# Performance work log

Hardware: AMD Instinct MI355X
Metric: run time of the kernel (lower is better)

## Reference

```python
import jax, jax.numpy as jnp
import numpy as np
import math

NUM_HEADS = 16
NUM_KV_HEADS = 4
HEAD_DIM = 128
ROPE_THETA = 10000.0


def rotate_half(x):
    half = x.shape[-1] // 2
    return jnp.concatenate((-x[..., half:], x[..., :half]), axis=-1)


def setup_inputs() -> dict:
    key = jax.random.key(0)
    ks = jax.random.split(key, 5)
    B, S, H = 2, 2048, 2048
    hidden_states = jax.random.normal(ks[0], (B, S, H), dtype=jnp.float32)
    scale = 1.0 / math.sqrt(H)
    wq = jax.random.normal(ks[1], (NUM_HEADS * HEAD_DIM, H), dtype=jnp.float32) * scale
    wk = jax.random.normal(ks[2], (NUM_KV_HEADS * HEAD_DIM, H), dtype=jnp.float32) * scale
    wv = jax.random.normal(ks[3], (NUM_KV_HEADS * HEAD_DIM, H), dtype=jnp.float32) * scale
    wo = jax.random.normal(ks[4], (H, NUM_HEADS * HEAD_DIM), dtype=jnp.float32) * scale
    # additive causal mask [B,1,S,S]
    causal = jnp.where(jnp.tril(jnp.ones((S, S), dtype=bool)), 0.0, -1e9).astype(jnp.float32)
    attention_mask = jnp.broadcast_to(causal[None, None], (B, 1, S, S))
    position_ids = jnp.broadcast_to(jnp.arange(S, dtype=jnp.int64)[None], (B, S))
    return {
        'hidden_states': hidden_states, 'wq': wq, 'wk': wk, 'wv': wv, 'wo': wo,
        'attention_mask': attention_mask, 'position_ids': position_ids,
    }


def reference(hidden_states, wq, wk, wv, wo, attention_mask, position_ids):
    B, S, H = hidden_states.shape
    nh, nkv, hd = NUM_HEADS, NUM_KV_HEADS, HEAD_DIM
    groups = nh // nkv

    # projections (torch Linear: x @ W^T)
    q = (hidden_states @ wq.T).reshape(B, S, nh, hd).transpose(0, 2, 1, 3)   # [B,nh,S,hd]
    k = (hidden_states @ wk.T).reshape(B, S, nkv, hd).transpose(0, 2, 1, 3)  # [B,nkv,S,hd]
    v = (hidden_states @ wv.T).reshape(B, S, nkv, hd).transpose(0, 2, 1, 3)

    # RoPE: cos/sin gathered by position_ids -> [B,1,S,hd]
    inv_freq = 1.0 / (ROPE_THETA ** (jnp.arange(0, hd, 2, dtype=jnp.float32) / hd))  # [hd/2]
    freqs = position_ids.astype(jnp.float32)[:, :, None] * inv_freq                  # [B,S,hd/2]
    emb = jnp.concatenate((freqs, freqs), axis=-1)                                   # [B,S,hd]
    cos = jnp.cos(emb)[:, None]
    sin = jnp.sin(emb)[:, None]
    q = q * cos + rotate_half(q) * sin
    k = k * cos + rotate_half(k) * sin

    # GQA: repeat kv heads
    k = jnp.repeat(k, groups, axis=1)  # [B,nh,S,hd]
    v = jnp.repeat(v, groups, axis=1)

    scores = jnp.einsum('bhqd,bhkd->bhqk', q, k) / math.sqrt(hd) + attention_mask
    attn = jax.nn.softmax(scores.astype(jnp.float32), axis=-1).astype(q.dtype)
    ctx = jnp.einsum('bhqk,bhkd->bhqd', attn, v)            # [B,nh,S,hd]
    ctx = ctx.transpose(0, 2, 1, 3).reshape(B, S, nh * hd)  # [B,S,H]
    out = ctx @ wo.T
    return out
```

## Files before the change

### kernel.cpp

```cpp
#include <hip/hip_runtime.h>
#include <hip/hip_bf16.h>
#include <stdint.h>

typedef __bf16 bf16x8 __attribute__((ext_vector_type(8)));
typedef float f32x4 __attribute__((ext_vector_type(4)));
typedef float f32x16 __attribute__((ext_vector_type(16)));

#define NH 16
#define NKV 4
#define HD 128
#define HQ (NH*HD)
#define HKV (NKV*HD)
#define LDX 3072

__device__ __forceinline__ void gl_lds16(const void* g, void* l) {
  __builtin_amdgcn_global_load_lds(
      (const __attribute__((address_space(1))) void*)g,
      (__attribute__((address_space(3))) void*)l, 16, 0, 0);
}

__device__ __forceinline__ uint32_t pk2(float lo, float hi) {
  union { __hip_bfloat16 h[2]; uint32_t u; } x;
  x.h[0] = __float2bfloat16(lo);
  x.h[1] = __float2bfloat16(hi);
  return x.u;
}

__global__ void k_cast_all(const float* __restrict__ hs, const float* __restrict__ wq,
                           const float* __restrict__ wk, const float* __restrict__ wv,
                           const float* __restrict__ wo,
                           __hip_bfloat16* __restrict__ Xb, __hip_bfloat16* __restrict__ Wqb,
                           __hip_bfloat16* __restrict__ Wkb, __hip_bfloat16* __restrict__ Wvb,
                           __hip_bfloat16* __restrict__ Wob) {
  int i = blockIdx.x * blockDim.x + threadIdx.x;
  const float* src; __hip_bfloat16* dst; int off;
  if (i < 2097152)      { src = hs; dst = Xb;  off = i; }
  else if (i < 3145728) { src = wq; dst = Wqb; off = i - 2097152; }
  else if (i < 3407872) { src = wk; dst = Wkb; off = i - 3145728; }
  else if (i < 3670016) { src = wv; dst = Wvb; off = i - 3407872; }
  else                  { src = wo; dst = Wob; off = i - 3670016; }
  float4 v = reinterpret_cast<const float4*>(src)[off];
  union { __hip_bfloat16 b[4]; ushort4 u; } o;
  o.b[0] = __float2bfloat16(v.x); o.b[1] = __float2bfloat16(v.y);
  o.b[2] = __float2bfloat16(v.z); o.b[3] = __float2bfloat16(v.w);
  reinterpret_cast<ushort4*>(dst)[off] = o.u;
}

__global__ void k_rope_vt(__hip_bfloat16* __restrict__ X, __hip_bfloat16* __restrict__ Vt,
                          const int* __restrict__ pid, int S) {
  __shared__ __hip_bfloat16 tile[32][33];
  const int RB = 20480;
  if (blockIdx.x < RB) {
    int idx = blockIdx.x * 256 + threadIdx.x;
    int i = idx & 63;
    int hh = (idx >> 6) % 20;
    int tok = idx / (20 * 64);
    bool is64 = (pid[1] == 0);
    int pos = is64 ? pid[2 * tok] : pid[tok];
    float f = (float)pos * __expf(-(float)i * (9.210340371976184f / 64.0f));
    float sn, cs;
    __sincosf(f, &sn, &cs);
    size_t base = (size_t)tok * LDX + hh * 128;
    float x0 = __bfloat162float(X[base + i]);
    float x1 = __bfloat162float(X[base + 64 + i]);
    X[base + i]      = __float2bfloat16(x0 * cs - x1 * sn);
    X[base + 64 + i] = __float2bfloat16(x1 * cs + x0 * sn);
  } else {
    int bb = blockIdx.x - RB;
    int bkv = bb >> 8;
    int rem = bb & 255;
    int s0 = (rem & 63) * 32, d0 = (rem >> 6) * 32;
    int b = bkv >> 2, kvh = bkv & 3;
    int tx = threadIdx.x & 31, ty = threadIdx.x >> 5;
    for (int i = 0; i < 32; i += 8)
      tile[ty + i][tx] = X[((size_t)(b * S) + s0 + ty + i) * LDX + 2560 + kvh * 128 + d0 + tx];
    __syncthreads();
    for (int i = 0; i < 32; i += 8)
      Vt[((size_t)bkv * 128 + d0 + ty + i) * S + s0 + tx] = tile[tx][ty + i];
  }
}

__global__ __launch_bounds__(512, 2) void k_gemm256(
    const __hip_bfloat16* __restrict__ A,
    const __hip_bfloat16* __restrict__ Bq,
    const __hip_bfloat16* __restrict__ Bk,
    const __hip_bfloat16* __restrict__ Bv,
    __hip_bfloat16* __restrict__ C, int Nld, int K, int nbm) {
  __shared__ __hip_bfloat16 As[2][2][256 * 32];
  __shared__ __hip_bfloat16 Bs[2][2][256 * 32];

  const int t = threadIdx.x, w = t >> 6, l = t & 63;
  const int lr = l & 15, lg = l >> 4;
  const int wr = w >> 2, wc = w & 3;

  const int nwg = gridDim.x;
  const int bid = blockIdx.x;
  const int cpx = nwg >> 3;
  const int id2 = (bid & 7) * cpx + (bid >> 3);
  const int bm = id2 % nbm, bn = id2 / nbm;

  const __hip_bfloat16* Ap = A + (size_t)(bm * 256) * K;
  const __hip_bfloat16* Bp;
  if (bn < 8)       Bp = Bq + (size_t)(bn * 256) * K;
  else if (bn < 10) Bp = Bk + (size_t)((bn - 8) * 256) * K;
  else              Bp = Bv + (size_t)((bn - 10) * 256) * K;

  auto stageHalf = [&](const __hip_bfloat16* gp, __hip_bfloat16* lp, int kt, int kk) {
#pragma unroll
    for (int inst = 0; inst < 2; ++inst) {
      const int chunk = inst * 512 + t;
      const int row = chunk >> 2, c = chunk & 3;
      gl_lds16(gp + (size_t)row * K + kt * 64 + kk * 32 + c * 8,
               lp + (size_t)(inst * 512 + (w << 6)) * 8);
    }
  };

  f32x4 acc[8][4] = {};
  const int nt = K >> 6;

  stageHalf(Ap, As[0][0], 0, 0);
  stageHalf(Bp, Bs[0][0], 0, 0);
  stageHalf(Ap, As[0][1], 0, 1);
  stageHalf(Bp, Bs[0][1], 0, 1);
  stageHalf(Ap, As[1][0], 1, 0);
  stageHalf(Bp, Bs[1][0], 1, 0);
  asm volatile("s_waitcnt vmcnt(4)" ::: "memory");
  __builtin_amdgcn_s_barrier();
  asm volatile("" ::: "memory");

  for (int tt = 0; tt < nt; ++tt) {
    const int cur = tt & 1;
    const int nx1 = (tt + 1 < nt) ? tt + 1 : nt - 1;
    const int nx2 = (tt + 2 < nt) ? tt + 2 : nt - 1;
    bf16x8 bF[4];
#pragma unroll
    for (int ph = 0; ph < 4; ++ph) {
      const int kk = ph >> 1, mh = ph & 1;
      bf16x8 aF[4];
      if (mh == 0) {
#pragma unroll
        for (int n = 0; n < 4; ++n)
          bF[n] = *reinterpret_cast<const bf16x8*>(
              &Bs[cur][kk][(wc * 64 + n * 16 + lr) * 32 + lg * 8]);
      }
#pragma unroll
      for (int m = 0; m < 4; ++m)
        aF[m] = *reinterpret_cast<const bf16x8*>(
            &As[cur][kk][(wr * 128 + mh * 64 + m * 16 + lr) * 32 + lg * 8]);
      if (ph == 0)      stageHalf(Ap, As[nx1 & 1][1], nx1, 1);
      else if (ph == 1) stageHalf(Bp, Bs[nx1 & 1][1], nx1, 1);
      else if (ph == 2) stageHalf(Ap, As[nx2 & 1][0], nx2, 0);
      else              stageHalf(Bp, Bs[nx2 & 1][0], nx2, 0);
      asm volatile("" ::: "memory");
      __builtin_amdgcn_s_barrier();
      asm volatile("" ::: "memory");
      __builtin_amdgcn_s_setprio(1);
#pragma unroll
      for (int m = 0; m < 4; ++m)
#pragma unroll
        for (int n = 0; n < 4; ++n)
          acc[mh * 4 + m][n] = __builtin_amdgcn_mfma_f32_16x16x32_bf16(
              aF[m], bF[n], acc[mh * 4 + m][n], 0, 0, 0);
      __builtin_amdgcn_s_setprio(0);
      if (ph == 3) asm volatile("s_waitcnt vmcnt(4)" ::: "memory");
      asm volatile("" ::: "memory");
      __builtin_amdgcn_s_barrier();
      asm volatile("" ::: "memory");
    }
  }

  const int row0 = bm * 256 + wr * 128;
  const int col0 = bn * 256 + wc * 64;
#pragma unroll
  for (int m = 0; m < 8; ++m)
#pragma unroll
    for (int n = 0; n < 4; ++n)
#pragma unroll
      for (int r = 0; r < 4; ++r)
        C[(size_t)(row0 + m * 16 + lg * 4 + r) * Nld + col0 + n * 16 + lr] =
            __float2bfloat16(acc[m][n][r]);
}

__global__ __launch_bounds__(512, 1) void k_gemmO(
    const __hip_bfloat16* __restrict__ A, const __hip_bfloat16* __restrict__ B,
    float* __restrict__ C, int N, int K) {
  __shared__ __hip_bfloat16 As[2][2][128 * 32];
  __shared__ __hip_bfloat16 Bs[2][2][256 * 32];

  const int t = threadIdx.x, w = t >> 6, l = t & 63;
  const int lr = l & 15, lg = l >> 4;
  const int wr = w >> 2, wc = w & 3;

  const int bid = blockIdx.x;
  const int id2 = (bid & 7) * 32 + (bid >> 3);
  const int bm = id2 & 31, bn = id2 >> 5;

  const __hip_bfloat16* Ap = A + (size_t)(bm * 128) * K;
  const __hip_bfloat16* Bp = B + (size_t)(bn * 256) * K;

  auto stageA = [&](__hip_bfloat16* lp, int kt, int kk) {
    const int row = t >> 2, c = t & 3;
    gl_lds16(Ap + (size_t)row * K + kt * 64 + kk * 32 + c * 8,
             lp + (size_t)(w << 6) * 8);
  };
  auto stageB = [&](__hip_bfloat16* lp, int kt, int kk) {
#pragma unroll
    for (int inst = 0; inst < 2; ++inst) {
      const int chunk = inst * 512 + t;
      const int row = chunk >> 2, c = chunk & 3;
      gl_lds16(Bp + (size_t)row * K + kt * 64 + kk * 32 + c * 8,
               lp + (size_t)(inst * 512 + (w << 6)) * 8);
    }
  };

  f32x4 acc[4][4] = {};
  const int nt = K >> 6;

  stageA(As[0][0], 0, 0);
  stageB(Bs[0][0], 0, 0);
  stageA(As[0][1], 0, 1);
  stageB(Bs[0][1], 0, 1);
  stageA(As[1][0], 1, 0);
  stageB(Bs[1][0], 1, 0);
  asm volatile("s_waitcnt vmcnt(3)" ::: "memory");
  __builtin_amdgcn_s_barrier();
  asm volatile("" ::: "memory");

  for (int tt = 0; tt < nt; ++tt) {
    const int cur = tt & 1;
    const int nx1 = (tt + 1 < nt) ? tt + 1 : nt - 1;
    const int nx2 = (tt + 2 < nt) ? tt + 2 : nt - 1;
    bf16x8 bF[4];
#pragma unroll
    for (int ph = 0; ph < 4; ++ph) {
      const int kk = ph >> 1, mh = ph & 1;
      bf16x8 aF[2];
      if (mh == 0) {
#pragma unroll
        for (int n = 0; n < 4; ++n)
          bF[n] = *reinterpret_cast<const bf16x8*>(
              &Bs[cur][kk][(wc * 64 + n * 16 + lr) * 32 + lg * 8]);
      }
#pragma unroll
      for (int m2 = 0; m2 < 2; ++m2)
        aF[m2] = *reinterpret_cast<const bf16x8*>(
            &As[cur][kk][(wr * 64 + mh * 32 + m2 * 16 + lr) * 32 + lg * 8]);
      if (ph == 0)      stageA(As[nx1 & 1][1], nx1, 1);
      else if (ph == 1) stageB(Bs[nx1 & 1][1], nx1, 1);
      else if (ph == 2) stageA(As[nx2 & 1][0], nx2, 0);
      else              stageB(Bs[nx2 & 1][0], nx2, 0);
      asm volatile("" ::: "memory");
      __builtin_amdgcn_s_barrier();
      asm volatile("" ::: "memory");
      __builtin_amdgcn_s_setprio(1);
#pragma unroll
      for (int m2 = 0; m2 < 2; ++m2)
#pragma unroll
        for (int n = 0; n < 4; ++n)
          acc[mh * 2 + m2][n] = __builtin_amdgcn_mfma_f32_16x16x32_bf16(
              aF[m2], bF[n], acc[mh * 2 + m2][n], 0, 0, 0);
      __builtin_amdgcn_s_setprio(0);
      if (ph == 3) asm volatile("s_waitcnt vmcnt(3)" ::: "memory");
      asm volatile("" ::: "memory");
      __builtin_amdgcn_s_barrier();
      asm volatile("" ::: "memory");
    }
  }

  const int row0 = bm * 128 + wr * 64;
  const int col0 = bn * 256 + wc * 64;
#pragma unroll
  for (int m = 0; m < 4; ++m)
#pragma unroll
    for (int n = 0; n < 4; ++n)
#pragma unroll
      for (int r = 0; r < 4; ++r)
        C[(size_t)(row0 + m * 16 + lg * 4 + r) * N + col0 + n * 16 + lr] =
            acc[m][n][r];
}

__global__ __launch_bounds__(256, 2) void k_attn(
    const __hip_bfloat16* __restrict__ X, const __hip_bfloat16* __restrict__ Vt,
    __hip_bfloat16* __restrict__ ctx, int S) {
  __shared__ __hip_bfloat16 SM[32768];

  const int bid = blockIdx.x;
  const int g  = bid & 7;
  const int idx = bid >> 3;
  int hi, jj;
  if (idx < 32) { hi = idx >> 4;              jj = idx & 15; }
  else          { hi = 2 + ((idx - 32) >> 4); jj = 15 - ((idx - 32) & 15); }
  const int b = g >> 2, kvh = g & 3;
  const int h = kvh * 4 + hi;

  const int t = threadIdx.x, w = t >> 6, l = t & 63;
  const int q = l & 31, hf = l >> 5;
  const int qt64 = (w < 2) ? jj : (31 - jj);
  const int q0w = qt64 * 64 + (w & 1) * 32;
  const int nt = 32 - jj;
  const float c1 = 0.12752511f;
  const float M0 = 48.0f;

  const __hip_bfloat16* Qp = X + ((size_t)(b * S) + q0w + q) * LDX + h * 128 + hf * 8;
  bf16x8 aq[8];
#pragma unroll
  for (int m = 0; m < 8; ++m)
    aq[m] = *reinterpret_cast<const bf16x8*>(Qp + m * 16);

  const __hip_bfloat16* KG = X + (size_t)(b * S) * LDX + 2048 + kvh * 128;
  const __hip_bfloat16* VG = Vt + ((size_t)(b * NKV + kvh) * 128) * S;

  auto stageK = [&](int buf, int kv0) {
#pragma unroll
    for (int j = 0; j < 4; ++j) {
      int off16 = (w * 4 + j) * 64 + l;
      int row = off16 >> 4;
      int c_nat = (off16 & 15) ^ (row & 7);
      gl_lds16(KG + (size_t)(kv0 + row) * LDX + c_nat * 8,
               &SM[buf * 8192 + (w * 4 + j) * 512]);
    }
  };
  auto stageV = [&](int buf, int kv0) {
#pragma unroll
    for (int j = 0; j < 4; ++j) {
      int off16 = (w * 4 + j) * 64 + l;
      int d = off16 >> 3;
      int c_nat = (off16 & 7) ^ (d & 7);
      gl_lds16(VG + (size_t)d * S + kv0 + c_nat * 8,
               &SM[16384 + buf * 8192 + (w * 4 + j) * 512]);
    }
  };

  f32x16 O[4] = {};
  float l_i = 0.0f;

  stageK(0, 0); stageV(0, 0);
  int cur = 0;
  for (int tkv = 0; tkv < nt; ++tkv) {
    const int kv0 = tkv * 64;
    if (tkv + 1 < nt) {
      stageK(cur ^ 1, kv0 + 64);
      stageV(cur ^ 1, kv0 + 64);
      asm volatile("s_waitcnt vmcnt(8)" ::: "memory");
    } else {
      asm volatile("s_waitcnt vmcnt(0)" ::: "memory");
    }
    __builtin_amdgcn_sched_barrier(0);
    __builtin_amdgcn_s_barrier();
    asm volatile("" ::: "memory");

    if (kv0 <= q0w + 31) {
      const __hip_bfloat16* Ksb = &SM[cur * 8192];
      const __hip_bfloat16* Vsb = &SM[16384 + cur * 8192];

      f32x16 p[2];
      __builtin_amdgcn_s_setprio(1);
#pragma unroll
      for (int sb = 0; sb < 2; ++sb) {
        f32x16 s0 = {}, s1 = {};
#pragma unroll
        for (int mm = 0; mm < 4; ++mm) {
          int arow = sb * 32 + q;
          int c0 = (4 * mm + hf) ^ (arow & 7);
          int c1i = (4 * mm + 2 + hf) ^ (arow & 7);
          bf16x8 kf0 = *reinterpret_cast<const bf16x8*>(&Ksb[arow * 128 + c0 * 8]);
          bf16x8 kf1 = *reinterpret_cast<const bf16x8*>(&Ksb[arow * 128 + c1i * 8]);
          s0 = __builtin_amdgcn_mfma_f32_32x32x16_bf16(kf0, aq[2 * mm], s0, 0, 0, 0);
          s1 = __builtin_amdgcn_mfma_f32_32x32x16_bf16(kf1, aq[2 * mm + 1], s1, 0, 0, 0);
        }
        p[sb] = s0 + s1;
      }
      __builtin_amdgcn_s_setprio(0);

      if (kv0 + 63 > q0w) {
#pragma unroll
        for (int sb = 0; sb < 2; ++sb)
#pragma unroll
          for (int r = 0; r < 16; ++r) {
            int kv_abs = kv0 + sb * 32 + (r & 3) + 8 * (r >> 2) + 4 * hf;
            if (kv_abs > q0w + q) p[sb][r] = -3.0e38f;
          }
      }

      float rs = 0.0f;
#pragma unroll
      for (int sb = 0; sb < 2; ++sb)
#pragma unroll
        for (int r = 0; r < 16; ++r) {
          float e = exp2f((p[sb][r] - M0) * c1);
          p[sb][r] = e;
          rs += e;
        }
      rs += __shfl_xor(rs, 32, 64);
      l_i += rs;

      uint32_t pku[2][8], swu[2][8];
#pragma unroll
      for (int sb = 0; sb < 2; ++sb)
#pragma unroll
        for (int gp = 0; gp < 4; ++gp) {
          pku[sb][gp * 2 + 0] = pk2(p[sb][gp * 4 + 0], p[sb][gp * 4 + 1]);
          pku[sb][gp * 2 + 1] = pk2(p[sb][gp * 4 + 2], p[sb][gp * 4 + 3]);
        }
#pragma unroll
      for (int sb = 0; sb < 2; ++sb)
#pragma unroll
        for (int ii = 0; ii < 8; ++ii)
          swu[sb][ii] = __shfl_xor((int)pku[sb][ii], 32, 64);

      __builtin_amdgcn_s_setprio(1);
#pragma unroll
      for (int kk = 0; kk < 4; ++kk) {
        const int sb = kk >> 1, bs = (kk & 1) * 4;
        union { uint32_t u[4]; bf16x8 v; } pf;
        pf.u[0] = hf ? swu[sb][bs + 2] : pku[sb][bs + 0];
        pf.u[1] = hf ? swu[sb][bs + 3] : pku[sb][bs + 1];
        pf.u[2] = hf ? pku[sb][bs + 2] : swu[sb][bs + 0];
        pf.u[3] = hf ? pku[sb][bs + 3] : swu[sb][bs + 1];
#pragma unroll
        for (int db = 0; db < 4; ++db) {
          int vrow = db * 32 + q;
          int c_lds = (2 * kk + hf) ^ (vrow & 7);
          bf16x8 vf = *reinterpret_cast<const bf16x8*>(&Vsb[vrow * 64 + c_lds * 8]);
          O[db] = __builtin_amdgcn_mfma_f32_32x32x16_bf16(vf, pf.v, O[db], 0, 0, 0);
        }
      }
      __builtin_amdgcn_s_setprio(0);
    }
    asm volatile("" ::: "memory");
    __builtin_amdgcn_s_barrier();
    asm volatile("" ::: "memory");
    cur ^= 1;
  }

  float inv = 1.0f / l_i;
  __hip_bfloat16* Lo = &SM[w * 4352];
#pragma unroll
  for (int db = 0; db < 4; ++db)
#pragma unroll
    for (int rr = 0; rr < 4; ++rr) {
      int d0 = db * 32 + rr * 8 + hf * 4;
      uint32_t u0 = pk2(O[db][rr * 4 + 0] * inv, O[db][rr * 4 + 1] * inv);
      uint32_t u1 = pk2(O[db][rr * 4 + 2] * inv, O[db][rr * 4 + 3] * inv);
      *reinterpret_cast<uint2*>(&Lo[q * 136 + d0]) = make_uint2(u0, u1);
    }
  __syncthreads();
#pragma unroll
  for (int it = 0; it < 8; ++it) {
    int row = it * 4 + (l >> 4), c = l & 15;
    bf16x8 vv = *reinterpret_cast<const bf16x8*>(&Lo[row * 136 + c * 8]);
    *reinterpret_cast<bf16x8*>(
        &ctx[((size_t)(b * S) + q0w + row) * HQ + h * 128 + c * 8]) = vv;
  }
}

extern "C" void kernel_launch(void* const* d_in, const int* in_sizes, int n_in,
                              void* d_out, int out_size, void* d_ws, size_t ws_size,
                              hipStream_t stream) {
  const int B = 2, S = 2048, H = 2048;
  const int M = B * S;

  const float* hs = (const float*)d_in[0];
  const float* wq = (const float*)d_in[1];
  const float* wk = (const float*)d_in[2];
  const float* wv = (const float*)d_in[3];
  const float* wo = (const float*)d_in[4];
  const int* pid = (const int*)d_in[6];

  char* p = (char*)d_ws;
  auto carve = [&](size_t bytes) {
    void* r = (void*)p;
    p += (bytes + 255) & ~(size_t)255;
    return r;
  };
  __hip_bfloat16* Xb   = (__hip_bfloat16*)carve((size_t)M * H * 2);
  __hip_bfloat16* Wqb  = (__hip_bfloat16*)carve((size_t)HQ * H * 2);
  __hip_bfloat16* Wkb  = (__hip_bfloat16*)carve((size_t)HKV * H * 2);
  __hip_bfloat16* Wvb  = (__hip_bfloat16*)carve((size_t)HKV * H * 2);
  __hip_bfloat16* Wob  = (__hip_bfloat16*)carve((size_t)H * HQ * 2);
  __hip_bfloat16* XQKV = (__hip_bfloat16*)carve((size_t)M * LDX * 2);
  __hip_bfloat16* Vtb  = (__hip_bfloat16*)carve((size_t)M * HKV * 2);
  __hip_bfloat16* Ctx  = (__hip_bfloat16*)carve((size_t)M * HQ * 2);

  k_cast_all<<<18432, 256, 0, stream>>>(hs, wq, wk, wv, wo, Xb, Wqb, Wkb, Wvb, Wob);

  k_gemm256<<<dim3(16 * 12), 512, 0, stream>>>(Xb, Wqb, Wkb, Wvb, XQKV, LDX, H, 16);

  k_rope_vt<<<dim3(20480 + 2048), 256, 0, stream>>>(XQKV, Vtb, pid, S);

  k_attn<<<dim3(512), 256, 0, stream>>>(XQKV, Vtb, Ctx, S);

  k_gemmO<<<dim3(256), 512, 0, stream>>>(Ctx, Wob, (float*)d_out, H, HQ);
}
```

Before: 253.4 us.

## Restructure attention blocks to two waves each handling 64 query rows

The attention kernel now launches 128-thread blocks with two waves, and each wave processes two 32-row query subtiles. Each K and V fragment read from LDS therefore feeds two MFMAs, halving LDS fragment traffic per FLOP. Query tiles are reassigned to 128-row blocks with an interleaved short/long ordering for causal load balance, and each wave stages twice as many K/V chunks. In exchange it doubles per-wave register pressure for accumulators and Q fragments, and it cuts threads per block, which may lower occupancy and latency hiding.

Result: slower. 293.2 us (+15.7%).

```diff
diff --git a/kernel.cpp b/kernel.cpp
--- a/kernel.cpp
+++ b/kernel.cpp
@@ -279,7 +279,7 @@
             acc[m][n][r];
 }
 
-__global__ __launch_bounds__(256, 2) void k_attn(
+__global__ __launch_bounds__(128, 1) void k_attn(
     const __hip_bfloat16* __restrict__ X, const __hip_bfloat16* __restrict__ Vt,
     __hip_bfloat16* __restrict__ ctx, int S) {
   __shared__ __hip_bfloat16 SM[32768];
@@ -287,52 +287,53 @@
   const int bid = blockIdx.x;
   const int g  = bid & 7;
   const int idx = bid >> 3;
-  int hi, jj;
-  if (idx < 32) { hi = idx >> 4;              jj = idx & 15; }
-  else          { hi = 2 + ((idx - 32) >> 4); jj = 15 - ((idx - 32) & 15); }
+  const int hi = idx >> 4;
+  const int m  = idx & 15;
+  const int k  = (m & 1) ? (15 - (m >> 1)) : (m >> 1);
   const int b = g >> 2, kvh = g & 3;
   const int h = kvh * 4 + hi;
 
   const int t = threadIdx.x, w = t >> 6, l = t & 63;
   const int q = l & 31, hf = l >> 5;
-  const int qt64 = (w < 2) ? jj : (31 - jj);
-  const int q0w = qt64 * 64 + (w & 1) * 32;
-  const int nt = 32 - jj;
+  const int q0w = k * 128 + w * 64;
+  const int nt = 2 * k + 2;
   const float c1 = 0.12752511f;
   const float M0 = 48.0f;
 
   const __hip_bfloat16* Qp = X + ((size_t)(b * S) + q0w + q) * LDX + h * 128 + hf * 8;
-  bf16x8 aq[8];
-#pragma unroll
-  for (int m = 0; m < 8; ++m)
-    aq[m] = *reinterpret_cast<const bf16x8*>(Qp + m * 16);
+  bf16x8 aq[2][8];
+#pragma unroll
+  for (int s = 0; s < 2; ++s)
+#pragma unroll
+    for (int mm = 0; mm < 8; ++mm)
+      aq[s][mm] = *reinterpret_cast<const bf16x8*>(Qp + (size_t)s * 32 * LDX + mm * 16);
 
   const __hip_bfloat16* KG = X + (size_t)(b * S) * LDX + 2048 + kvh * 128;
   const __hip_bfloat16* VG = Vt + ((size_t)(b * NKV + kvh) * 128) * S;
 
   auto stageK = [&](int buf, int kv0) {
 #pragma unroll
-    for (int j = 0; j < 4; ++j) {
-      int off16 = (w * 4 + j) * 64 + l;
+    for (int j = 0; j < 8; ++j) {
+      int off16 = (w * 8 + j) * 64 + l;
       int row = off16 >> 4;
       int c_nat = (off16 & 15) ^ (row & 7);
       gl_lds16(KG + (size_t)(kv0 + row) * LDX + c_nat * 8,
-               &SM[buf * 8192 + (w * 4 + j) * 512]);
+               &SM[buf * 8192 + (w * 8 + j) * 512]);
     }
   };
   auto stageV = [&](int buf, int kv0) {
 #pragma unroll
-    for (int j = 0; j < 4; ++j) {
-      int off16 = (w * 4 + j) * 64 + l;
+    for (int j = 0; j < 8; ++j) {
+      int off16 = (w * 8 + j) * 64 + l;
       int d = off16 >> 3;
       int c_nat = (off16 & 7) ^ (d & 7);
       gl_lds16(VG + (size_t)d * S + kv0 + c_nat * 8,
-               &SM[16384 + buf * 8192 + (w * 4 + j) * 512]);
+               &SM[16384 + buf * 8192 + (w * 8 + j) * 512]);
     }
   };
 
-  f32x16 O[4] = {};
-  float l_i = 0.0f;
+  f32x16 O[2][4] = {};
+  float l_i[2] = {0.0f, 0.0f};
 
   stageK(0, 0); stageV(0, 0);
   int cur = 0;
@@ -341,7 +342,7 @@
     if (tkv + 1 < nt) {
       stageK(cur ^ 1, kv0 + 64);
       stageV(cur ^ 1, kv0 + 64);
-      asm volatile("s_waitcnt vmcnt(8)" ::: "memory");
+      asm volatile("s_waitcnt vmcnt(16)" ::: "memory");
     } else {
       asm volatile("s_waitcnt vmcnt(0)" ::: "memory");
     }
@@ -349,80 +350,93 @@
     __builtin_amdgcn_s_barrier();
     asm volatile("" ::: "memory");
 
-    if (kv0 <= q0w + 31) {
+    if (kv0 <= q0w + 63) {
       const __hip_bfloat16* Ksb = &SM[cur * 8192];
       const __hip_bfloat16* Vsb = &SM[16384 + cur * 8192];
 
-      f32x16 p[2];
+      f32x16 p[2][2];
       __builtin_amdgcn_s_setprio(1);
 #pragma unroll
       for (int sb = 0; sb < 2; ++sb) {
         f32x16 s0 = {}, s1 = {};
-#pragma unroll
-        for (int mm = 0; mm < 4; ++mm) {
-          int arow = sb * 32 + q;
-          int c0 = (4 * mm + hf) ^ (arow & 7);
-          int c1i = (4 * mm + 2 + hf) ^ (arow & 7);
-          bf16x8 kf0 = *reinterpret_cast<const bf16x8*>(&Ksb[arow * 128 + c0 * 8]);
-          bf16x8 kf1 = *reinterpret_cast<const bf16x8*>(&Ksb[arow * 128 + c1i * 8]);
-          s0 = __builtin_amdgcn_mfma_f32_32x32x16_bf16(kf0, aq[2 * mm], s0, 0, 0, 0);
-          s1 = __builtin_amdgcn_mfma_f32_32x32x16_bf16(kf1, aq[2 * mm + 1], s1, 0, 0, 0);
+        const int arow = sb * 32 + q;
+#pragma unroll
+        for (int mm = 0; mm < 8; ++mm) {
+          int c_lds = (2 * mm + hf) ^ (q & 7);
+          bf16x8 kf = *reinterpret_cast<const bf16x8*>(&Ksb[arow * 128 + c_lds * 8]);
+          s0 = __builtin_amdgcn_mfma_f32_32x32x16_bf16(kf, aq[0][mm], s0, 0, 0, 0);
+          s1 = __builtin_amdgcn_mfma_f32_32x32x16_bf16(kf, aq[1][mm], s1, 0, 0, 0);
         }
-        p[sb] = s0 + s1;
+        p[0][sb] = s0;
+        p[1][sb] = s1;
       }
       __builtin_amdgcn_s_setprio(0);
 
-      if (kv0 + 63 > q0w) {
+#pragma unroll
+      for (int s = 0; s < 2; ++s) {
+        if (kv0 + 63 > q0w + s * 32) {
+#pragma unroll
+          for (int sb = 0; sb < 2; ++sb)
+#pragma unroll
+            for (int r = 0; r < 16; ++r) {
+              int kv_abs = kv0 + sb * 32 + (r & 3) + 8 * (r >> 2) + 4 * hf;
+              if (kv_abs > q0w + s * 32 + q) p[s][sb][r] = -3.0e38f;
+            }
+        }
+      }
+
+#pragma unroll
+      for (int s = 0; s < 2; ++s) {
+        float rs = 0.0f;
 #pragma unroll
         for (int sb = 0; sb < 2; ++sb)
 #pragma unroll
           for (int r = 0; r < 16; ++r) {
-            int kv_abs = kv0 + sb * 32 + (r & 3) + 8 * (r >> 2) + 4 * hf;
-            if (kv_abs > q0w + q) p[sb][r] = -3.0e38f;
+            float e = exp2f((p[s][sb][r] - M0) * c1);
+            p[s][sb][r] = e;
+            rs += e;
           }
-      }
-
-      float rs = 0.0f;
-#pragma unroll
-      for (int sb = 0; sb < 2; ++sb)
-#pragma unroll
-        for (int r = 0; r < 16; ++r) {
-          float e = exp2f((p[sb][r] - M0) * c1);
-          p[sb][r] = e;
-          rs += e;
-        }
-      rs += __shfl_xor(rs, 32, 64);
-      l_i += rs;
-
-      uint32_t pku[2][8], swu[2][8];
-#pragma unroll
-      for (int sb = 0; sb < 2; ++sb)
-#pragma unroll
-        for (int gp = 0; gp < 4; ++gp) {
-          pku[sb][gp * 2 + 0] = pk2(p[sb][gp * 4 + 0], p[sb][gp * 4 + 1]);
-          pku[sb][gp * 2 + 1] = pk2(p[sb][gp * 4 + 2], p[sb][gp * 4 + 3]);
-        }
-#pragma unroll
-      for (int sb = 0; sb < 2; ++sb)
-#pragma unroll
-        for (int ii = 0; ii < 8; ++ii)
-          swu[sb][ii] = __shfl_xor((int)pku[sb][ii], 32, 64);
+        rs += __shfl_xor(rs, 32, 64);
+        l_i[s] += rs;
+      }
+
+      uint32_t pku[2][2][8], swu[2][2][8];
+#pragma unroll
+      for (int s = 0; s < 2; ++s)
+#pragma unroll
+        for (int sb = 0; sb < 2; ++sb)
+#pragma unroll
+          for (int gp = 0; gp < 4; ++gp) {
+            pku[s][sb][gp * 2 + 0] = pk2(p[s][sb][gp * 4 + 0], p[s][sb][gp * 4 + 1]);
+            pku[s][sb][gp * 2 + 1] = pk2(p[s][sb][gp * 4 + 2], p[s][sb][gp * 4 + 3]);
+          }
+#pragma unroll
+      for (int s = 0; s < 2; ++s)
+#pragma unroll
+        for (int sb = 0; sb < 2; ++sb)
+#pragma unroll
+          for (int ii = 0; ii < 8; ++ii)
+            swu[s][sb][ii] = __shfl_xor((int)pku[s][sb][ii], 32, 64);
 
       __builtin_amdgcn_s_setprio(1);
 #pragma unroll
       for (int kk = 0; kk < 4; ++kk) {
         const int sb = kk >> 1, bs = (kk & 1) * 4;
-        union { uint32_t u[4]; bf16x8 v; } pf;
-        pf.u[0] = hf ? swu[sb][bs + 2] : pku[sb][bs + 0];
-        pf.u[1] = hf ? swu[sb][bs + 3] : pku[sb][bs + 1];
-        pf.u[2] = hf ? pku[sb][bs + 2] : swu[sb][bs + 0];
-        pf.u[3] = hf ? pku[sb][bs + 3] : swu[sb][bs + 1];
+        union { uint32_t u[4]; bf16x8 v; } pf[2];
+#pragma unroll
+        for (int s = 0; s < 2; ++s) {
+          pf[s].u[0] = hf ? swu[s][sb][bs + 2] : pku[s][sb][bs + 0];
+          pf[s].u[1] = hf ? swu[s][sb][bs + 3] : pku[s][sb][bs + 1];
+          pf[s].u[2] = hf ? pku[s][sb][bs + 2] : swu[s][sb][bs + 0];
+          pf[s].u[3] = hf ? pku[s][sb][bs + 3] : swu[s][sb][bs + 1];
+        }
 #pragma unroll
         for (int db = 0; db < 4; ++db) {
           int vrow = db * 32 + q;
-          int c_lds = (2 * kk + hf) ^ (vrow & 7);
+          int c_lds = (2 * kk + hf) ^ (q & 7);
           bf16x8 vf = *reinterpret_cast<const bf16x8*>(&Vsb[vrow * 64 + c_lds * 8]);
-          O[db] = __builtin_amdgcn_mfma_f32_32x32x16_bf16(vf, pf.v, O[db], 0, 0, 0);
+          O[0][db] = __builtin_amdgcn_mfma_f32_32x32x16_bf16(vf, pf[0].v, O[0][db], 0, 0, 0);
+          O[1][db] = __builtin_amdgcn_mfma_f32_32x32x16_bf16(vf, pf[1].v, O[1][db], 0, 0, 0);
         }
       }
       __builtin_amdgcn_s_setprio(0);
@@ -433,24 +447,28 @@
     cur ^= 1;
   }
 
-  float inv = 1.0f / l_i;
-  __hip_bfloat16* Lo = &SM[w * 4352];
-#pragma unroll
-  for (int db = 0; db < 4; ++db)
-#pragma unroll
-    for (int rr = 0; rr < 4; ++rr) {
-      int d0 = db * 32 + rr * 8 + hf * 4;
-      uint32_t u0 = pk2(O[db][rr * 4 + 0] * inv, O[db][rr * 4 + 1] * inv);
-      uint32_t u1 = pk2(O[db][rr * 4 + 2] * inv, O[db][rr * 4 + 3] * inv);
-      *reinterpret_cast<uint2*>(&Lo[q * 136 + d0]) = make_uint2(u0, u1);
-    }
-  __syncthreads();
-#pragma unroll
-  for (int it = 0; it < 8; ++it) {
-    int row = it * 4 + (l >> 4), c = l & 15;
-    bf16x8 vv = *reinterpret_cast<const bf16x8*>(&Lo[row * 136 + c * 8]);
-    *reinterpret_cast<bf16x8*>(
-        &ctx[((size_t)(b * S) + q0w + row) * HQ + h * 128 + c * 8]) = vv;
+#pragma unroll
+  for (int s = 0; s < 2; ++s) {
+    float inv = 1.0f / l_i[s];
+    __hip_bfloat16* Lo = &SM[w * 4352];
+    __syncthreads();
+#pragma unroll
+    for (int db = 0; db < 4; ++db)
+#pragma unroll
+      for (int rr = 0; rr < 4; ++rr) {
+        int d0 = db * 32 + rr * 8 + hf * 4;
+        uint32_t u0 = pk2(O[s][db][rr * 4 + 0] * inv, O[s][db][rr * 4 + 1] * inv);
+        uint32_t u1 = pk2(O[s][db][rr * 4 + 2] * inv, O[s][db][rr * 4 + 3] * inv);
+        *reinterpret_cast<uint2*>(&Lo[q * 136 + d0]) = make_uint2(u0, u1);
+      }
+    __syncthreads();
+#pragma unroll
+    for (int it = 0; it < 8; ++it) {
+      int row = it * 4 + (l >> 4), c = l & 15;
+      bf16x8 vv = *reinterpret_cast<const bf16x8*>(&Lo[row * 136 + c * 8]);
+      *reinterpret_cast<bf16x8*>(
+          &ctx[((size_t)(b * S) + q0w + s * 32 + row) * HQ + h * 128 + c * 8]) = vv;
+    }
   }
 }
 
@@ -488,7 +506,7 @@
 
   k_rope_vt<<<dim3(20480 + 2048), 256, 0, stream>>>(XQKV, Vtb, pid, S);
 
-  k_attn<<<dim3(512), 256, 0, stream>>>(XQKV, Vtb, Ctx, S);
+  k_attn<<<dim3(512), 128, 0, stream>>>(XQKV, Vtb, Ctx, S);
 
   k_gemmO<<<dim3(256), 512, 0, stream>>>(Ctx, Wob, (float*)d_out, H, HQ);
 }
```

## Retile QKV projection GEMM to 128x384 blocks filling all CUs

Applied to the files above, without the earlier changes.

The fused QKV projection GEMM changes from 256x256 output tiles (192 workgroups) to 128x384 tiles (256 workgroups). The goal is one workgroup per CU so no compute units sit idle during the projection. The kernel now reads the Q, K and V weights through a single pointer, which relies on those buffers being carved contiguously in the workspace. Each wave now holds a 64x96 accumulator with 6 B fragments and 2 A fragments per phase, and the load-wait counts were reworked to match the 1+3 loads per stage. The trade-off is a smaller M tile, which gives lower arithmetic intensity per workgroup, and occupancy drops to one block per CU.

Result: slower. 273.4 us (+7.9%).

```diff
diff --git a/kernel.cpp b/kernel.cpp
--- a/kernel.cpp
+++ b/kernel.cpp
@@ -80,50 +80,47 @@
   }
 }
 
-__global__ __launch_bounds__(512, 2) void k_gemm256(
-    const __hip_bfloat16* __restrict__ A,
-    const __hip_bfloat16* __restrict__ Bq,
-    const __hip_bfloat16* __restrict__ Bk,
-    const __hip_bfloat16* __restrict__ Bv,
-    __hip_bfloat16* __restrict__ C, int Nld, int K, int nbm) {
-  __shared__ __hip_bfloat16 As[2][2][256 * 32];
-  __shared__ __hip_bfloat16 Bs[2][2][256 * 32];
+__global__ __launch_bounds__(512, 1) void k_gemmQKV(
+    const __hip_bfloat16* __restrict__ A, const __hip_bfloat16* __restrict__ B,
+    __hip_bfloat16* __restrict__ C, int Nld, int K) {
+  __shared__ __hip_bfloat16 As[2][2][128 * 32];
+  __shared__ __hip_bfloat16 Bs[2][2][384 * 32];
 
   const int t = threadIdx.x, w = t >> 6, l = t & 63;
   const int lr = l & 15, lg = l >> 4;
   const int wr = w >> 2, wc = w & 3;
 
-  const int nwg = gridDim.x;
   const int bid = blockIdx.x;
-  const int cpx = nwg >> 3;
-  const int id2 = (bid & 7) * cpx + (bid >> 3);
-  const int bm = id2 % nbm, bn = id2 / nbm;
-
-  const __hip_bfloat16* Ap = A + (size_t)(bm * 256) * K;
-  const __hip_bfloat16* Bp;
-  if (bn < 8)       Bp = Bq + (size_t)(bn * 256) * K;
-  else if (bn < 10) Bp = Bk + (size_t)((bn - 8) * 256) * K;
-  else              Bp = Bv + (size_t)((bn - 10) * 256) * K;
-
-  auto stageHalf = [&](const __hip_bfloat16* gp, __hip_bfloat16* lp, int kt, int kk) {
-#pragma unroll
-    for (int inst = 0; inst < 2; ++inst) {
+  const int id2 = (bid & 7) * 32 + (bid >> 3);
+  const int bm = id2 & 31, bn = id2 >> 5;
+
+  const __hip_bfloat16* Ap = A + (size_t)(bm * 128) * K;
+  const __hip_bfloat16* Bp = B + (size_t)(bn * 384) * K;
+
+  auto stageA = [&](__hip_bfloat16* lp, int kt, int kk) {
+    const int row = t >> 2, c = t & 3;
+    gl_lds16(Ap + (size_t)row * K + kt * 64 + kk * 32 + c * 8,
+             lp + (size_t)(w << 6) * 8);
+  };
+  auto stageB = [&](__hip_bfloat16* lp, int kt, int kk) {
+#pragma unroll
+    for (int inst = 0; inst < 3; ++inst) {
       const int chunk = inst * 512 + t;
       const int row = chunk >> 2, c = chunk & 3;
-      gl_lds16(gp + (size_t)row * K + kt * 64 + kk * 32 + c * 8,
+      gl_lds16(Bp + (size_t)row * K + kt * 64 + kk * 32 + c * 8,
                lp + (size_t)(inst * 512 + (w << 6)) * 8);
     }
   };
 
-  f32x4 acc[8][4] = {};
+  f32x4 acc[4][6] = {};
   const int nt = K >> 6;
 
-  stageHalf(Ap, As[0][0], 0, 0);
-  stageHalf(Bp, Bs[0][0], 0, 0);
-  stageHalf(Ap, As[0][1], 0, 1);
-  stageHalf(Bp, Bs[0][1], 0, 1);
-  stageHalf(Ap, As[1][0], 1, 0);
-  stageHalf(Bp, Bs[1][0], 1, 0);
+  stageA(As[0][0], 0, 0);
+  stageB(Bs[0][0], 0, 0);
+  stageA(As[0][1], 0, 1);
+  stageB(Bs[0][1], 0, 1);
+  stageA(As[1][0], 1, 0);
+  stageB(Bs[1][0], 1, 0);
   asm volatile("s_waitcnt vmcnt(4)" ::: "memory");
   __builtin_amdgcn_s_barrier();
   asm volatile("" ::: "memory");
@@ -132,35 +129,35 @@
     const int cur = tt & 1;
     const int nx1 = (tt + 1 < nt) ? tt + 1 : nt - 1;
     const int nx2 = (tt + 2 < nt) ? tt + 2 : nt - 1;
-    bf16x8 bF[4];
+    bf16x8 bF[6];
 #pragma unroll
     for (int ph = 0; ph < 4; ++ph) {
       const int kk = ph >> 1, mh = ph & 1;
-      bf16x8 aF[4];
+      bf16x8 aF[2];
       if (mh == 0) {
 #pragma unroll
-        for (int n = 0; n < 4; ++n)
+        for (int n = 0; n < 6; ++n)
           bF[n] = *reinterpret_cast<const bf16x8*>(
-              &Bs[cur][kk][(wc * 64 + n * 16 + lr) * 32 + lg * 8]);
+              &Bs[cur][kk][(wc * 96 + n * 16 + lr) * 32 + lg * 8]);
       }
 #pragma unroll
-      for (int m = 0; m < 4; ++m)
-        aF[m] = *reinterpret_cast<const bf16x8*>(
-            &As[cur][kk][(wr * 128 + mh * 64 + m * 16 + lr) * 32 + lg * 8]);
-      if (ph == 0)      stageHalf(Ap, As[nx1 & 1][1], nx1, 1);
-      else if (ph == 1) stageHalf(Bp, Bs[nx1 & 1][1], nx1, 1);
-      else if (ph == 2) stageHalf(Ap, As[nx2 & 1][0], nx2, 0);
-      else              stageHalf(Bp, Bs[nx2 & 1][0], nx2, 0);
+      for (int m2 = 0; m2 < 2; ++m2)
+        aF[m2] = *reinterpret_cast<const bf16x8*>(
+            &As[cur][kk][(wr * 64 + mh * 32 + m2 * 16 + lr) * 32 + lg * 8]);
+      if (ph == 0)      stageA(As[nx1 & 1][1], nx1, 1);
+      else if (ph == 1) stageB(Bs[nx1 & 1][1], nx1, 1);
+      else if (ph == 2) stageA(As[nx2 & 1][0], nx2, 0);
+      else              stageB(Bs[nx2 & 1][0], nx2, 0);
       asm volatile("" ::: "memory");
       __builtin_amdgcn_s_barrier();
       asm volatile("" ::: "memory");
       __builtin_amdgcn_s_setprio(1);
 #pragma unroll
-      for (int m = 0; m < 4; ++m)
-#pragma unroll
-        for (int n = 0; n < 4; ++n)
-          acc[mh * 4 + m][n] = __builtin_amdgcn_mfma_f32_16x16x32_bf16(
-              aF[m], bF[n], acc[mh * 4 + m][n], 0, 0, 0);
+      for (int m2 = 0; m2 < 2; ++m2)
+#pragma unroll
+        for (int n = 0; n < 6; ++n)
+          acc[mh * 2 + m2][n] = __builtin_amdgcn_mfma_f32_16x16x32_bf16(
+              aF[m2], bF[n], acc[mh * 2 + m2][n], 0, 0, 0);
       __builtin_amdgcn_s_setprio(0);
       if (ph == 3) asm volatile("s_waitcnt vmcnt(4)" ::: "memory");
       asm volatile("" ::: "memory");
@@ -169,12 +166,12 @@
     }
   }
 
-  const int row0 = bm * 256 + wr * 128;
-  const int col0 = bn * 256 + wc * 64;
-#pragma unroll
-  for (int m = 0; m < 8; ++m)
-#pragma unroll
-    for (int n = 0; n < 4; ++n)
+  const int row0 = bm * 128 + wr * 64;
+  const int col0 = bn * 384 + wc * 96;
+#pragma unroll
+  for (int m = 0; m < 4; ++m)
+#pragma unroll
+    for (int n = 0; n < 6; ++n)
 #pragma unroll
       for (int r = 0; r < 4; ++r)
         C[(size_t)(row0 + m * 16 + lg * 4 + r) * Nld + col0 + n * 16 + lr] =
@@ -484,7 +481,7 @@
 
   k_cast_all<<<18432, 256, 0, stream>>>(hs, wq, wk, wv, wo, Xb, Wqb, Wkb, Wvb, Wob);
 
-  k_gemm256<<<dim3(16 * 12), 512, 0, stream>>>(Xb, Wqb, Wkb, Wvb, XQKV, LDX, H, 16);
+  k_gemmQKV<<<dim3(256), 512, 0, stream>>>(Xb, Wqb, XQKV, LDX, H);
 
   k_rope_vt<<<dim3(20480 + 2048), 256, 0, stream>>>(XQKV, Vtb, pid, S);
 
```
